# Optimization experiments

Measured on AMD Instinct MI355X. Metric: run time of the kernel, lower is better.

The kernel has to match this reference:

```python
import jax, jax.numpy as jnp
import numpy as np

B, N, D, K = 8, 4096, 128, 1024


def setup_inputs() -> dict:
    key = jax.random.key(0)
    kx, kp = jax.random.split(key)
    x = jax.random.normal(kx, (B, N, D), dtype=jnp.float32)
    # matches nn.Parameter(...).uniform_(-0.1, 0.1)
    prototypes = jax.random.uniform(kp, (K, D), dtype=jnp.float32, minval=-0.1, maxval=0.1)
    return {"x": x, "prototypes": prototypes, "hard": 1}


def reference(x, prototypes, hard):
    x_sq = jnp.sum(x * x, axis=-1, keepdims=True)            # [B,N,1]
    p_sq = jnp.sum(prototypes * prototypes, axis=-1)         # [K]
    xp = jnp.einsum('bnd,kd->bnk', x, prototypes)            # [B,N,K]
    scores = -(x_sq + p_sq[None, None, :] - 2.0 * xp)        # [B,N,K]
    if bool(hard):
        idx = jnp.argmax(scores, axis=-1)                    # [B,N]
        matched = prototypes[idx]                            # [B,N,D]
    else:
        w = jax.nn.softmax(scores, axis=-1)                  # [B,N,K]
        matched = jnp.einsum('bnk,kd->bnd', w, prototypes)   # [B,N,D]
    return (matched, scores)
```

## Files before the change

### kernel.cpp

```cpp
#include <hip/hip_runtime.h>

typedef short short8 __attribute__((ext_vector_type(8)));
typedef float f32x4  __attribute__((ext_vector_type(4)));

constexpr int M_TOT  = 8 * 4096;
constexpr int K_PROT = 1024;
constexpr int D_DIM  = 128;

constexpr size_t WS_PF_OFF = (size_t)K_PROT * 4;

__device__ inline unsigned short bf16_hi(float f) {
  unsigned u = __builtin_bit_cast(unsigned, f);
  unsigned r = u + 0x7FFFu + ((u >> 16) & 1u);
  return (unsigned short)(r >> 16);
}
__device__ inline float bf16_tof(unsigned short h) {
  return __builtin_bit_cast(float, (unsigned)h << 16);
}

__device__ inline void barrier_lds() {
  asm volatile("s_waitcnt lgkmcnt(0)\n\ts_barrier" ::: "memory");
}

__global__ __launch_bounds__(256) void psq_kernel(
    const float* __restrict__ p, float* __restrict__ psq) {
  int group = blockIdx.x * 8 + (threadIdx.x >> 5);
  int lane  = threadIdx.x & 31;
  if (group >= K_PROT) return;
  float4 v = reinterpret_cast<const float4*>(p + (size_t)group * D_DIM)[lane];
  float s = v.x * v.x + v.y * v.y + v.z * v.z + v.w * v.w;
  #pragma unroll
  for (int off = 16; off > 0; off >>= 1) s += __shfl_down(s, off, 32);
  if (lane == 0) psq[group] = s;
}

__global__ __launch_bounds__(256) void pfrag_kernel(
    const float* __restrict__ p, short* __restrict__ pf) {
  int g    = blockIdx.x * 256 + threadIdx.x;
  int lane = g & 63;
  int s    = (g >> 6) & 7;
  int ng   = g >> 9;
  int part = s >> 2, ks = s & 3;
  int proto = ng * 16 + (lane & 15);
  int k0    = ks * 32 + (lane >> 4) * 8;
  const float4* pr = (const float4*)(p + (size_t)proto * D_DIM + k0);
  float4 a = pr[0], b = pr[1];
  float e[8] = {a.x, a.y, a.z, a.w, b.x, b.y, b.z, b.w};
  short8 frag;
  #pragma unroll
  for (int j = 0; j < 8; ++j) {
    unsigned short h = bf16_hi(e[j]);
    if (part) h = bf16_hi(e[j] - bf16_tof(h));
    frag[j] = (short)h;
  }
  *(short8*)(pf + (size_t)g * 8) = frag;
}

__global__ __launch_bounds__(256, 3) void proto_mfma(
    const float* __restrict__ x, const float* __restrict__ p,
    const short* __restrict__ pf, const float* __restrict__ psq,
    float* __restrict__ matched, float* __restrict__ scores) {
  __shared__ short xlds[32 * 64 * 8];
  __shared__ float sbuf[16][260];
  __shared__ float sv[4][64];
  __shared__ int   si[4][64];
  __shared__ int   fidx[64];
  __shared__ float xsqv[64];

  const int tid = threadIdx.x;
  const int w   = tid >> 6;
  const int l   = tid & 63;
  const int m0  = blockIdx.x * 64;

  float (*xpart)[16] = (float(*)[16])&sbuf[0][0];

  #pragma unroll
  for (int i = 0; i < 8; ++i) {
    int piece = i * 256 + tid;
    int s = piece >> 6;
    int ks = s & 3, nt = (s >> 2) & 3, part = s >> 4;
    int pix = m0 + nt * 16 + (l & 15);
    int k0  = ks * 32 + (l >> 4) * 8;
    const float4* xr = (const float4*)(x + (size_t)pix * D_DIM + k0);
    float4 a = xr[0], b = xr[1];
    float e[8] = {a.x, a.y, a.z, a.w, b.x, b.y, b.z, b.w};
    if (part == 0) {
      float ss = e[0]*e[0] + e[1]*e[1] + e[2]*e[2] + e[3]*e[3]
               + e[4]*e[4] + e[5]*e[5] + e[6]*e[6] + e[7]*e[7];
      xpart[nt * 16 + (l & 15)][ks * 4 + (l >> 4)] = ss;
    }
    short8 frag;
    #pragma unroll
    for (int j = 0; j < 8; ++j) {
      unsigned short h = bf16_hi(e[j]);
      if (part) h = bf16_hi(e[j] - bf16_tof(h));
      frag[j] = (short)h;
    }
    *(short8*)(xlds + (size_t)piece * 8) = frag;
  }
  __syncthreads();

  if (tid < 64) {
    float s = 0.f;
    #pragma unroll
    for (int j = 0; j < 16; ++j) s += xpart[tid][j];
    xsqv[tid] = s;
  }
  __syncthreads();

  float xs[4];
  #pragma unroll
  for (int nt = 0; nt < 4; ++nt) xs[nt] = xsqv[nt * 16 + (l & 15)];

  float best[4]; int bidx[4];
  #pragma unroll
  for (int nt = 0; nt < 4; ++nt) { best[nt] = -3.4e38f; bidx[nt] = 0; }

  for (int chunk = 0; chunk < 4; ++chunk) {
    f32x4 acc[4][4];
    #pragma unroll
    for (int mt = 0; mt < 4; ++mt)
      #pragma unroll
      for (int nt = 0; nt < 4; ++nt) acc[mt][nt] = (f32x4){0.f, 0.f, 0.f, 0.f};

    const int pgbase = chunk * 16 + w * 4;

    #pragma unroll
    for (int ks = 0; ks < 4; ++ks) {
      short8 pah[4], pal[4], bh[4], bl[4];
      #pragma unroll
      for (int mt = 0; mt < 4; ++mt) {
        pah[mt] = *(const short8*)(pf + ((size_t)((pgbase + mt) * 8 + ks) * 64 + l) * 8);
        pal[mt] = *(const short8*)(pf + ((size_t)((pgbase + mt) * 8 + 4 + ks) * 64 + l) * 8);
      }
      #pragma unroll
      for (int nt = 0; nt < 4; ++nt) {
        bh[nt] = *(const short8*)(xlds + (size_t)(((nt * 4 + ks) * 64) + l) * 8);
        bl[nt] = *(const short8*)(xlds + (size_t)(((16 + nt * 4 + ks) * 64) + l) * 8);
      }
      #pragma unroll
      for (int mt = 0; mt < 4; ++mt)
        #pragma unroll
        for (int nt = 0; nt < 4; ++nt)
          acc[mt][nt] = __builtin_amdgcn_mfma_f32_16x16x32_bf16(pah[mt], bh[nt], acc[mt][nt], 0, 0, 0);
      #pragma unroll
      for (int mt = 0; mt < 4; ++mt)
        #pragma unroll
        for (int nt = 0; nt < 4; ++nt)
          acc[mt][nt] = __builtin_amdgcn_mfma_f32_16x16x32_bf16(pah[mt], bl[nt], acc[mt][nt], 0, 0, 0);
      #pragma unroll
      for (int mt = 0; mt < 4; ++mt)
        #pragma unroll
        for (int nt = 0; nt < 4; ++nt)
          acc[mt][nt] = __builtin_amdgcn_mfma_f32_16x16x32_bf16(pal[mt], bh[nt], acc[mt][nt], 0, 0, 0);
    }

    #pragma unroll
    for (int mt = 0; mt < 4; ++mt) {
      int pbase = chunk * 256 + w * 64 + mt * 16 + (l >> 4) * 4;
      float psa[4];
      *(float4*)psa = *(const float4*)(psq + pbase);
      #pragma unroll
      for (int nt = 0; nt < 4; ++nt) {
        f32x4 o;
        {
          #pragma clang fp contract(off)
          #pragma unroll
          for (int r = 0; r < 4; ++r) {
            float s = xs[nt] + psa[r];
            o[r] = __builtin_fmaf(2.0f, acc[mt][nt][r], -s);
            if (o[r] > best[nt]) { best[nt] = o[r]; bidx[nt] = pbase + r; }
          }
        }
        acc[mt][nt] = o;
      }
    }

    #pragma unroll
    for (int r = 0; r < 4; ++r) {
      #pragma unroll
      for (int mt = 0; mt < 4; ++mt)
        *(f32x4*)&sbuf[l & 15][(w << 6) + mt * 16 + ((l >> 4) << 2)] = acc[mt][r];
      barrier_lds();
      #pragma unroll
      for (int ps = 0; ps < 4; ++ps) {
        int row = ps * 4 + w;
        f32x4 v = *(const f32x4*)&sbuf[row][l << 2];
        __builtin_nontemporal_store(v,
            (f32x4*)(scores + (size_t)(m0 + r * 16 + row) * K_PROT + chunk * 256) + l);
      }
      barrier_lds();
    }
  }

  #pragma unroll
  for (int nt = 0; nt < 4; ++nt) {
    #pragma unroll
    for (int m = 16; m <= 32; m <<= 1) {
      float ov = __shfl_xor(best[nt], m);
      int   oi = __shfl_xor(bidx[nt], m);
      if (ov > best[nt] || (ov == best[nt] && oi < bidx[nt])) {
        best[nt] = ov; bidx[nt] = oi;
      }
    }
  }
  if (l < 16) {
    #pragma unroll
    for (int nt = 0; nt < 4; ++nt) {
      sv[w][nt * 16 + l] = best[nt];
      si[w][nt * 16 + l] = bidx[nt];
    }
  }
  __syncthreads();
  if (tid < 64) {
    float v = sv[0][tid]; int bi = si[0][tid];
    #pragma unroll
    for (int e = 1; e < 4; ++e) {
      float vv = sv[e][tid]; int ii = si[e][tid];
      if (vv > v || (vv == v && ii < bi)) { v = vv; bi = ii; }
    }
    fidx[tid] = bi;
  }
  __syncthreads();

  for (int q = tid; q < 64 * 32; q += 256) {
    int pix = q >> 5, f4 = q & 31;
    float4 v = ((const float4*)(p + (size_t)fidx[pix] * D_DIM))[f4];
    __builtin_nontemporal_store(*(f32x4*)&v,
        (f32x4*)(matched + (size_t)(m0 + pix) * D_DIM) + f4);
  }
}

extern "C" void kernel_launch(void* const* d_in, const int* in_sizes, int n_in,
                              void* d_out, int out_size, void* d_ws, size_t ws_size,
                              hipStream_t stream) {
  const float* x = (const float*)d_in[0];
  const float* p = (const float*)d_in[1];

  float* matched = (float*)d_out;
  float* scores  = (float*)d_out + (size_t)M_TOT * D_DIM;

  float* psq = (float*)d_ws;
  short* pf  = (short*)((char*)d_ws + WS_PF_OFF);

  psq_kernel<<<K_PROT / 8, 256, 0, stream>>>(p, psq);
  pfrag_kernel<<<128, 256, 0, stream>>>(p, pf);
  proto_mfma<<<M_TOT / 64, 256, 0, stream>>>(x, p, pf, psq, matched, scores);
}
```

Measured before the change: 207.7 us.

## Shrink pixel tile to 16 rows per block and stage scores in wider LDS buffer

```diff
diff --git a/kernel.cpp b/kernel.cpp
--- a/kernel.cpp
+++ b/kernel.cpp
@@ -56,51 +56,48 @@
   *(short8*)(pf + (size_t)g * 8) = frag;
 }
 
-__global__ __launch_bounds__(256, 3) void proto_mfma(
+__global__ __launch_bounds__(256, 2) void proto_mfma(
     const float* __restrict__ x, const float* __restrict__ p,
     const short* __restrict__ pf, const float* __restrict__ psq,
     float* __restrict__ matched, float* __restrict__ scores) {
-  __shared__ short xlds[32 * 64 * 8];
-  __shared__ float sbuf[16][260];
-  __shared__ float sv[4][64];
-  __shared__ int   si[4][64];
-  __shared__ int   fidx[64];
-  __shared__ float xsqv[64];
+  __shared__ short xlds[8 * 64 * 8];
+  __shared__ float sbuf[16][520];
+  __shared__ float sv[4][16];
+  __shared__ int   si[4][16];
+  __shared__ int   fidx[16];
+  __shared__ float xsqv[16];
 
   const int tid = threadIdx.x;
   const int w   = tid >> 6;
   const int l   = tid & 63;
-  const int m0  = blockIdx.x * 64;
+  const int m0  = blockIdx.x * 16;
 
   float (*xpart)[16] = (float(*)[16])&sbuf[0][0];
 
   #pragma unroll
-  for (int i = 0; i < 8; ++i) {
-    int piece = i * 256 + tid;
-    int s = piece >> 6;
-    int ks = s & 3, nt = (s >> 2) & 3, part = s >> 4;
-    int pix = m0 + nt * 16 + (l & 15);
-    int k0  = ks * 32 + (l >> 4) * 8;
+  for (int i = 0; i < 2; ++i) {
+    int pix = m0 + (l & 15);
+    int k0  = w * 32 + (l >> 4) * 8;
     const float4* xr = (const float4*)(x + (size_t)pix * D_DIM + k0);
     float4 a = xr[0], b = xr[1];
     float e[8] = {a.x, a.y, a.z, a.w, b.x, b.y, b.z, b.w};
-    if (part == 0) {
+    if (i == 0) {
       float ss = e[0]*e[0] + e[1]*e[1] + e[2]*e[2] + e[3]*e[3]
                + e[4]*e[4] + e[5]*e[5] + e[6]*e[6] + e[7]*e[7];
-      xpart[nt * 16 + (l & 15)][ks * 4 + (l >> 4)] = ss;
+      xpart[l & 15][w * 4 + (l >> 4)] = ss;
     }
     short8 frag;
     #pragma unroll
     for (int j = 0; j < 8; ++j) {
       unsigned short h = bf16_hi(e[j]);
-      if (part) h = bf16_hi(e[j] - bf16_tof(h));
+      if (i) h = bf16_hi(e[j] - bf16_tof(h));
       frag[j] = (short)h;
     }
-    *(short8*)(xlds + (size_t)piece * 8) = frag;
+    *(short8*)(xlds + (size_t)((i * 4 + w) * 64 + l) * 8) = frag;
   }
   __syncthreads();
 
-  if (tid < 64) {
+  if (tid < 16) {
     float s = 0.f;
     #pragma unroll
     for (int j = 0; j < 16; ++j) s += xpart[tid][j];
@@ -108,111 +105,83 @@
   }
   __syncthreads();
 
-  float xs[4];
-  #pragma unroll
-  for (int nt = 0; nt < 4; ++nt) xs[nt] = xsqv[nt * 16 + (l & 15)];
-
-  float best[4]; int bidx[4];
-  #pragma unroll
-  for (int nt = 0; nt < 4; ++nt) { best[nt] = -3.4e38f; bidx[nt] = 0; }
-
-  for (int chunk = 0; chunk < 4; ++chunk) {
-    f32x4 acc[4][4];
-    #pragma unroll
-    for (int mt = 0; mt < 4; ++mt)
+  const float xs = xsqv[l & 15];
+
+  float best = -3.4e38f;
+  int   bidx = 0;
+
+  for (int half = 0; half < 2; ++half) {
+    #pragma unroll
+    for (int ci = 0; ci < 2; ++ci) {
+      const int chunk  = half * 2 + ci;
+      const int pgbase = chunk * 16 + w * 4;
+
+      f32x4 acc[4];
       #pragma unroll
-      for (int nt = 0; nt < 4; ++nt) acc[mt][nt] = (f32x4){0.f, 0.f, 0.f, 0.f};
-
-    const int pgbase = chunk * 16 + w * 4;
-
-    #pragma unroll
-    for (int ks = 0; ks < 4; ++ks) {
-      short8 pah[4], pal[4], bh[4], bl[4];
+      for (int mt = 0; mt < 4; ++mt) acc[mt] = (f32x4){0.f, 0.f, 0.f, 0.f};
+
+      #pragma unroll
+      for (int ks = 0; ks < 4; ++ks) {
+        short8 pah[4], pal[4];
+        #pragma unroll
+        for (int mt = 0; mt < 4; ++mt) {
+          pah[mt] = *(const short8*)(pf + ((size_t)((pgbase + mt) * 8 + ks) * 64 + l) * 8);
+          pal[mt] = *(const short8*)(pf + ((size_t)((pgbase + mt) * 8 + 4 + ks) * 64 + l) * 8);
+        }
+        short8 bh = *(const short8*)(xlds + (size_t)((ks) * 64 + l) * 8);
+        short8 bl = *(const short8*)(xlds + (size_t)((4 + ks) * 64 + l) * 8);
+        #pragma unroll
+        for (int mt = 0; mt < 4; ++mt)
+          acc[mt] = __builtin_amdgcn_mfma_f32_16x16x32_bf16(pah[mt], bh, acc[mt], 0, 0, 0);
+        #pragma unroll
+        for (int mt = 0; mt < 4; ++mt)
+          acc[mt] = __builtin_amdgcn_mfma_f32_16x16x32_bf16(pah[mt], bl, acc[mt], 0, 0, 0);
+        #pragma unroll
+        for (int mt = 0; mt < 4; ++mt)
+          acc[mt] = __builtin_amdgcn_mfma_f32_16x16x32_bf16(pal[mt], bh, acc[mt], 0, 0, 0);
+      }
+
       #pragma unroll
       for (int mt = 0; mt < 4; ++mt) {
-        pah[mt] = *(const short8*)(pf + ((size_t)((pgbase + mt) * 8 + ks) * 64 + l) * 8);
-        pal[mt] = *(const short8*)(pf + ((size_t)((pgbase + mt) * 8 + 4 + ks) * 64 + l) * 8);
-      }
-      #pragma unroll
-      for (int nt = 0; nt < 4; ++nt) {
-        bh[nt] = *(const short8*)(xlds + (size_t)(((nt * 4 + ks) * 64) + l) * 8);
-        bl[nt] = *(const short8*)(xlds + (size_t)(((16 + nt * 4 + ks) * 64) + l) * 8);
-      }
-      #pragma unroll
-      for (int mt = 0; mt < 4; ++mt)
-        #pragma unroll
-        for (int nt = 0; nt < 4; ++nt)
-          acc[mt][nt] = __builtin_amdgcn_mfma_f32_16x16x32_bf16(pah[mt], bh[nt], acc[mt][nt], 0, 0, 0);
-      #pragma unroll
-      for (int mt = 0; mt < 4; ++mt)
-        #pragma unroll
-        for (int nt = 0; nt < 4; ++nt)
-          acc[mt][nt] = __builtin_amdgcn_mfma_f32_16x16x32_bf16(pah[mt], bl[nt], acc[mt][nt], 0, 0, 0);
-      #pragma unroll
-      for (int mt = 0; mt < 4; ++mt)
-        #pragma unroll
-        for (int nt = 0; nt < 4; ++nt)
-          acc[mt][nt] = __builtin_amdgcn_mfma_f32_16x16x32_bf16(pal[mt], bh[nt], acc[mt][nt], 0, 0, 0);
-    }
-
-    #pragma unroll
-    for (int mt = 0; mt < 4; ++mt) {
-      int pbase = chunk * 256 + w * 64 + mt * 16 + (l >> 4) * 4;
-      float psa[4];
-      *(float4*)psa = *(const float4*)(psq + pbase);
-      #pragma unroll
-      for (int nt = 0; nt < 4; ++nt) {
+        int pbase = chunk * 256 + w * 64 + mt * 16 + (l >> 4) * 4;
+        float psa[4];
+        *(float4*)psa = *(const float4*)(psq + pbase);
         f32x4 o;
         {
           #pragma clang fp contract(off)
           #pragma unroll
           for (int r = 0; r < 4; ++r) {
-            float s = xs[nt] + psa[r];
-            o[r] = __builtin_fmaf(2.0f, acc[mt][nt][r], -s);
-            if (o[r] > best[nt]) { best[nt] = o[r]; bidx[nt] = pbase + r; }
+            float s = xs + psa[r];
+            o[r] = __builtin_fmaf(2.0f, acc[mt][r], -s);
+            if (o[r] > best) { best = o[r]; bidx = pbase + r; }
           }
         }
-        acc[mt][nt] = o;
+        *(f32x4*)&sbuf[l & 15][pbase - half * 512] = o;
       }
     }
 
-    #pragma unroll
-    for (int r = 0; r < 4; ++r) {
-      #pragma unroll
-      for (int mt = 0; mt < 4; ++mt)
-        *(f32x4*)&sbuf[l & 15][(w << 6) + mt * 16 + ((l >> 4) << 2)] = acc[mt][r];
-      barrier_lds();
-      #pragma unroll
-      for (int ps = 0; ps < 4; ++ps) {
-        int row = ps * 4 + w;
-        f32x4 v = *(const f32x4*)&sbuf[row][l << 2];
-        __builtin_nontemporal_store(v,
-            (f32x4*)(scores + (size_t)(m0 + r * 16 + row) * K_PROT + chunk * 256) + l);
-      }
-      barrier_lds();
-    }
-  }
-
-  #pragma unroll
-  for (int nt = 0; nt < 4; ++nt) {
-    #pragma unroll
-    for (int m = 16; m <= 32; m <<= 1) {
-      float ov = __shfl_xor(best[nt], m);
-      int   oi = __shfl_xor(bidx[nt], m);
-      if (ov > best[nt] || (ov == best[nt] && oi < bidx[nt])) {
-        best[nt] = ov; bidx[nt] = oi;
-      }
-    }
-  }
-  if (l < 16) {
-    #pragma unroll
-    for (int nt = 0; nt < 4; ++nt) {
-      sv[w][nt * 16 + l] = best[nt];
-      si[w][nt * 16 + l] = bidx[nt];
-    }
-  }
-  __syncthreads();
-  if (tid < 64) {
+    barrier_lds();
+    #pragma unroll
+    for (int ps = 0; ps < 8; ++ps) {
+      int idx = ps * 256 + tid;
+      int row = idx >> 7;
+      int c4  = idx & 127;
+      f32x4 v = *(const f32x4*)&sbuf[row][c4 * 4];
+      __builtin_nontemporal_store(v,
+          (f32x4*)(scores + (size_t)(m0 + row) * K_PROT + half * 512) + c4);
+    }
+    barrier_lds();
+  }
+
+  #pragma unroll
+  for (int m = 16; m <= 32; m <<= 1) {
+    float ov = __shfl_xor(best, m);
+    int   oi = __shfl_xor(bidx, m);
+    if (ov > best || (ov == best && oi < bidx)) { best = ov; bidx = oi; }
+  }
+  if (l < 16) { sv[w][l] = best; si[w][l] = bidx; }
+  barrier_lds();
+  if (tid < 16) {
     float v = sv[0][tid]; int bi = si[0][tid];
     #pragma unroll
     for (int e = 1; e < 4; ++e) {
@@ -221,9 +190,11 @@
     }
     fidx[tid] = bi;
   }
-  __syncthreads();
-
-  for (int q = tid; q < 64 * 32; q += 256) {
+  barrier_lds();
+
+  #pragma unroll
+  for (int q0 = 0; q0 < 2; ++q0) {
+    int q = q0 * 256 + tid;
     int pix = q >> 5, f4 = q & 31;
     float4 v = ((const float4*)(p + (size_t)fidx[pix] * D_DIM))[f4];
     __builtin_nontemporal_store(*(f32x4*)&v,
@@ -245,5 +216,5 @@
 
   psq_kernel<<<K_PROT / 8, 256, 0, stream>>>(p, psq);
   pfrag_kernel<<<128, 256, 0, stream>>>(p, pf);
-  proto_mfma<<<M_TOT / 64, 256, 0, stream>>>(x, p, pf, psq, matched, scores);
-}
+  proto_mfma<<<M_TOT / 16, 256, 0, stream>>>(x, p, pf, psq, matched, scores);
+}
```

Result: no change. 207.1 us (-0.3%).
